# Optimization experiments

Hardware: AMD Instinct MI355X
Metric: run time of the kernel (lower is better)

Reference implementation:

```python
import jax, jax.numpy as jnp
import numpy as np

FD, FO, FK, H = 1024, 512, 128, 4
N = 32768


def setup_inputs() -> dict:
    key = jax.random.key(0)
    ks = jax.random.split(key, 8)
    s = 0.02
    return {
        "Xd": jax.random.normal(ks[0], (N, FD), dtype=jnp.float32),
        "Xo": jax.random.normal(ks[1], (N, FO), dtype=jnp.float32),
        "Wq": jax.random.normal(ks[2], (FO, FK * H), dtype=jnp.float32) * s,
        "bq": jnp.zeros((FK * H,), dtype=jnp.float32),
        "Wk": jax.random.normal(ks[3], (FD, FK * H), dtype=jnp.float32) * s,
        "bk": jnp.zeros((FK * H,), dtype=jnp.float32),
        "Wv": jax.random.normal(ks[4], (FD, FD * H), dtype=jnp.float32) * s,
        "bv": jnp.zeros((FD * H,), dtype=jnp.float32),
    }


def reference(Xd, Xo, Wq, bq, Wk, bk, Wv, bv):
    n = Xd.shape[0]
    Q = (Xo @ Wq + bq).reshape(n, H, FK)      # (n, H, fk)
    K = (Xd @ Wk + bk).reshape(n, H, FK)      # (n, H, fk)
    V = (Xd @ Wv + bv).reshape(n, H, FD)      # (n, H, fd)
    scores = jnp.sum(Q * K, axis=2, keepdims=True)  # (n, H, 1), no softmax
    Z = scores * V                              # (n, H, fd)
    Z = jnp.max(Z, axis=1)                      # max pooling over heads -> (n, fd)
    return Z  # dropout is identity in inference
```

## Files before the change

### kernel.cpp

```cpp
#include <hip/hip_runtime.h>

typedef __attribute__((ext_vector_type(8))) short short8;
typedef __attribute__((ext_vector_type(4))) float f32x4;

#define GLL16(gp, lp) __builtin_amdgcn_global_load_lds( \
    (__attribute__((address_space(1))) void*)(gp), \
    (__attribute__((address_space(3))) void*)(lp), 16, 0, 0)

__device__ __forceinline__ unsigned short f2b(float f) {
  unsigned int u = __builtin_bit_cast(unsigned int, f);
  u += 0x7fffu + ((u >> 16) & 1u);
  return (unsigned short)(u >> 16);
}
__device__ __forceinline__ float b2f(unsigned short s) {
  unsigned int u = ((unsigned int)s) << 16;
  return __builtin_bit_cast(float, u);
}

__global__ __launch_bounds__(256) void conv_k(const float* __restrict__ in,
                                              short8* __restrict__ out, long n8) {
  for (long i = (long)blockIdx.x * 256 + threadIdx.x; i < n8;
       i += (long)gridDim.x * 256) {
    const float4* p = (const float4*)in + 2 * i;
    float4 a = p[0], b = p[1];
    short8 v;
    v[0] = (short)f2b(a.x); v[1] = (short)f2b(a.y);
    v[2] = (short)f2b(a.z); v[3] = (short)f2b(a.w);
    v[4] = (short)f2b(b.x); v[5] = (short)f2b(b.y);
    v[6] = (short)f2b(b.z); v[7] = (short)f2b(b.w);
    out[i] = v;
  }
}

__global__ __launch_bounds__(256) void tconv_k(const float* __restrict__ in,
                                               unsigned short* __restrict__ out,
                                               int K, int C, int inter) {
  __shared__ float t[32][33];
  int k0 = blockIdx.x * 32, c0 = blockIdx.y * 32;
  int tx = threadIdx.x & 31, ty = threadIdx.x >> 5;
#pragma unroll
  for (int p = 0; p < 4; ++p)
    t[ty + p * 8][tx] = in[(size_t)(k0 + ty + p * 8) * C + c0 + tx];
  __syncthreads();
#pragma unroll
  for (int p = 0; p < 4; ++p) {
    int c = ty + p * 8;
    int gc = c0 + c;
    int orow = inter ? ((gc & 1023) * 4 + (gc >> 10)) : gc;
    out[(size_t)orow * K + k0 + tx] = f2b(t[tx][c]);
  }
}

template <int KD>
__global__ __launch_bounds__(512, 2) void gemm_v256_k(
    const unsigned short* __restrict__ A, const unsigned short* __restrict__ Bt,
    const float* __restrict__ bias, const float* __restrict__ sc,
    float* __restrict__ Z) {
  __shared__ __align__(16) char lds[65536];
  __shared__ float s_sc[1024];

  const int NKT = KD / 32;
  int tid = threadIdx.x;
  int bid = blockIdx.x;
  int cpx = gridDim.x >> 3;
  int lb = (bid & 7) * cpx + (bid >> 3);
  int mtile = lb >> 4, nt0 = lb & 15;
  long m0 = (long)mtile * 256;
  int l = tid & 63, wid = tid >> 6, wm = wid >> 2, wn = wid & 3;

  for (int i = tid; i < 1024; i += 512) s_sc[i] = sc[m0 * 4 + i];

  int srg = tid >> 3, slot = tid & 7;
  int se = slot ^ (srg & 7);
  int par = se >> 2, kc = se & 3;
  int rowb = srg * 2 + par;
  const char* aT = (const char*)(A + m0 * KD) + (long)rowb * (KD * 2) + kc * 16;
  const char* bT = (const char*)(Bt + (long)nt0 * 256 * KD) + (long)rowb * (KD * 2) + kc * 16;
  char* ldsb = (char*)lds;
  int dstOff = wid * 1024;

  auto stage = [&](int kt, int bb) {
    int ko = kt * 64;
    GLL16(aT + ko,                  ldsb + bb * 32768 + dstOff);
    GLL16(aT + 128 * (KD * 2) + ko, ldsb + bb * 32768 + 8192 + dstOff);
    GLL16(bT + ko,                  ldsb + bb * 32768 + 16384 + dstOff);
    GLL16(bT + 128 * (KD * 2) + ko, ldsb + bb * 32768 + 24576 + dstOff);
  };

  int ar = l & 15, kcl = l >> 4;
  int aoffR[8], boffR[4];
#pragma unroll
  for (int m = 0; m < 8; ++m) {
    int wr = wm * 128 + m * 16 + ar, sr = wr >> 1;
    aoffR[m] = sr * 128 + (((((wr & 1) << 2) | kcl) ^ (sr & 7)) << 4);
  }
#pragma unroll
  for (int n = 0; n < 4; ++n) {
    int br = wn * 64 + n * 16 + ar, sr = br >> 1;
    boffR[n] = sr * 128 + (((((br & 1) << 2) | kcl) ^ (sr & 7)) << 4);
  }

  f32x4 zero = {0.f, 0.f, 0.f, 0.f};
  f32x4 acc[8][4];
#pragma unroll
  for (int m = 0; m < 8; ++m)
#pragma unroll
    for (int n = 0; n < 4; ++n) acc[m][n] = zero;

  stage(0, 0);

  for (int t = 0; t < NKT; ++t) {
    asm volatile("s_waitcnt vmcnt(0)" ::: "memory");
    __builtin_amdgcn_s_barrier();
    asm volatile("" ::: "memory");
    if (t + 1 < NKT) stage(t + 1, (t + 1) & 1);

    const char* Al = ldsb + (t & 1) * 32768;
    const char* Bl = Al + 16384;
    short8 bf[4], af[4], af2[4];
#pragma unroll
    for (int n = 0; n < 4; ++n) bf[n] = *(const short8*)(Bl + boffR[n]);
#pragma unroll
    for (int m = 0; m < 4; ++m) af[m] = *(const short8*)(Al + aoffR[m]);
#pragma unroll
    for (int m = 0; m < 4; ++m) af2[m] = *(const short8*)(Al + aoffR[4 + m]);

#pragma unroll
    for (int m = 0; m < 4; ++m)
#pragma unroll
      for (int n = 0; n < 4; ++n)
        acc[m][n] = __builtin_amdgcn_mfma_f32_16x16x32_bf16(af[m], bf[n],
                                                            acc[m][n], 0, 0, 0);
#pragma unroll
    for (int m = 0; m < 4; ++m)
#pragma unroll
      for (int n = 0; n < 4; ++n)
        acc[4 + m][n] = __builtin_amdgcn_mfma_f32_16x16x32_bf16(af2[m], bf[n],
                                                                acc[4 + m][n], 0, 0, 0);
  }

  __syncthreads();
  float* Zs = (float*)ldsb;
#pragma unroll
  for (int n = 0; n < 4; ++n) {
    int pl = wn * 64 + n * 16 + (l & 15);
    int pg = nt0 * 256 + pl;
    int h = pl & 3;
    float bb = bias[(pg & 3) * 1024 + (pg >> 2)];
#pragma unroll
    for (int mi = 0; mi < 8; ++mi) {
      int rl = wm * 128 + mi * 16 + ((l >> 4) << 2);
#pragma unroll
      for (int r = 0; r < 4; ++r) {
        float z = s_sc[(rl + r) * 4 + h] * (acc[mi][n][r] + bb);
        z = fmaxf(z, __shfl_xor(z, 1));
        z = fmaxf(z, __shfl_xor(z, 2));
        if ((l & 3) == 0) Zs[(rl + r) * 64 + (pl >> 2)] = z;
      }
    }
  }
  __syncthreads();
#pragma unroll
  for (int it = 0; it < 8; ++it) {
    int i = it * 512 + tid;
    int row = i >> 4, d4 = i & 15;
    f32x4 v = *(const f32x4*)&Zs[row * 64 + d4 * 4];
    *(f32x4*)&Z[(m0 + row) * 1024 + nt0 * 64 + d4 * 4] = v;
  }
}

template <int KD, int EPI>
__global__ __launch_bounds__(256) void gemm_k(
    const unsigned short* __restrict__ A, const unsigned short* __restrict__ Bt,
    const float* __restrict__ bias, const unsigned short* __restrict__ Qb,
    unsigned short* __restrict__ outb, float* __restrict__ sc) {
  __shared__ __align__(16) unsigned short As[128 * 64];
  __shared__ __align__(16) unsigned short Bs[128 * 64];
  __shared__ float sred[128][2];

  int tid = threadIdx.x;
  int bid = blockIdx.x;
  int ntile = bid & 3, mtile = bid >> 2;
  int l = tid & 63, wid = tid >> 6, wm = wid >> 1, wn = wid & 1;
  int m0 = mtile * 128;

  const unsigned short* Ab = A + (size_t)m0 * KD;
  const unsigned short* Bb = Bt + (size_t)ntile * 128 * KD;

  f32x4 zero = {0.f, 0.f, 0.f, 0.f};
  f32x4 acc[4][4];
#pragma unroll
  for (int m = 0; m < 4; ++m)
#pragma unroll
    for (int n = 0; n < 4; ++n) acc[m][n] = zero;

  for (int kt = 0; kt < KD / 64; ++kt) {
    const unsigned short* sA = Ab + kt * 64;
    const unsigned short* sB = Bb + kt * 64;
#pragma unroll
    for (int p = 0; p < 4; ++p) {
      int row = p * 32 + wid * 8 + (l >> 3);
      int sch = (l & 7) ^ (row & 7);
      GLL16((const char*)(sA + (size_t)row * KD) + sch * 16,
            (char*)As + p * 4096 + wid * 1024);
    }
#pragma unroll
    for (int p = 0; p < 4; ++p) {
      int row = p * 32 + wid * 8 + (l >> 3);
      int sch = (l & 7) ^ (row & 7);
      GLL16((const char*)(sB + (size_t)row * KD) + sch * 16,
            (char*)Bs + p * 4096 + wid * 1024);
    }
    __syncthreads();
#pragma unroll
    for (int ks = 0; ks < 2; ++ks) {
      short8 af[4], bfr[4];
#pragma unroll
      for (int m = 0; m < 4; ++m) {
        int row = wm * 64 + m * 16 + (l & 15);
        int kc = ks * 4 + (l >> 4);
        af[m] = *(const short8*)((const char*)As + row * 128 +
                                 ((kc ^ (row & 7)) << 4));
      }
#pragma unroll
      for (int n = 0; n < 4; ++n) {
        int row = wn * 64 + n * 16 + (l & 15);
        int kc = ks * 4 + (l >> 4);
        bfr[n] = *(const short8*)((const char*)Bs + row * 128 +
                                  ((kc ^ (row & 7)) << 4));
      }
#pragma unroll
      for (int m = 0; m < 4; ++m)
#pragma unroll
        for (int n = 0; n < 4; ++n)
          acc[m][n] = __builtin_amdgcn_mfma_f32_16x16x32_bf16(af[m], bfr[n],
                                                              acc[m][n], 0, 0, 0);
    }
    __syncthreads();
  }

  if constexpr (EPI == 0) {
#pragma unroll
    for (int n = 0; n < 4; ++n) {
      int col = ntile * 128 + wn * 64 + n * 16 + (l & 15);
      float bb = bias[col];
#pragma unroll
      for (int m = 0; m < 4; ++m) {
        int rowb = m0 + wm * 64 + m * 16 + ((l >> 4) << 2);
#pragma unroll
        for (int r = 0; r < 4; ++r)
          outb[(size_t)(rowb + r) * 512 + col] = f2b(acc[m][n][r] + bb);
      }
    }
  } else {
    float part[4][4] = {};
#pragma unroll
    for (int n = 0; n < 4; ++n) {
      int col = ntile * 128 + wn * 64 + n * 16 + (l & 15);
      float bb = bias[col];
#pragma unroll
      for (int m = 0; m < 4; ++m) {
        int rowb = m0 + wm * 64 + m * 16 + ((l >> 4) << 2);
#pragma unroll
        for (int r = 0; r < 4; ++r) {
          float kv = acc[m][n][r] + bb;
          part[m][r] += kv * b2f(Qb[(size_t)(rowb + r) * 512 + col]);
        }
      }
    }
#pragma unroll
    for (int m = 0; m < 4; ++m)
#pragma unroll
      for (int r = 0; r < 4; ++r) {
        float s = part[m][r];
        s += __shfl_xor(s, 1);
        s += __shfl_xor(s, 2);
        s += __shfl_xor(s, 4);
        s += __shfl_xor(s, 8);
        if ((l & 15) == 0)
          sred[wm * 64 + m * 16 + ((l >> 4) << 2) + r][wn] = s;
      }
    __syncthreads();
    if (tid < 128) sc[(size_t)(m0 + tid) * 4 + ntile] = sred[tid][0] + sred[tid][1];
  }
}

__global__ __launch_bounds__(256) void naive_k(
    const float* __restrict__ Xd, const float* __restrict__ Xo,
    const float* __restrict__ Wq, const float* __restrict__ bq,
    const float* __restrict__ Wk, const float* __restrict__ bk,
    const float* __restrict__ Wv, const float* __restrict__ bv,
    float* __restrict__ Z) {
  int i = blockIdx.x, t = threadIdx.x;
  __shared__ float xd[1024], xo[512], s[4];
  for (int j = t; j < 1024; j += 256) xd[j] = Xd[(size_t)i * 1024 + j];
  for (int j = t; j < 512; j += 256) xo[j] = Xo[(size_t)i * 512 + j];
  if (t < 4) s[t] = 0.f;
  __syncthreads();
  for (int c = t; c < 512; c += 256) {
    float q = bq[c], k = bk[c];
    for (int j = 0; j < 512; ++j) q += xo[j] * Wq[(size_t)j * 512 + c];
    for (int j = 0; j < 1024; ++j) k += xd[j] * Wk[(size_t)j * 512 + c];
    atomicAdd(&s[c >> 7], q * k);
  }
  __syncthreads();
  for (int d = t; d < 1024; d += 256) {
    float z = -INFINITY;
    for (int h = 0; h < 4; ++h) {
      float v = bv[h * 1024 + d];
      for (int j = 0; j < 1024; ++j) v += xd[j] * Wv[(size_t)j * 4096 + h * 1024 + d];
      z = fmaxf(z, s[h] * v);
    }
    Z[(size_t)i * 1024 + d] = z;
  }
}

extern "C" void kernel_launch(void* const* d_in, const int* in_sizes, int n_in,
                              void* d_out, int out_size, void* d_ws, size_t ws_size,
                              hipStream_t stream) {
  const float* Xd = (const float*)d_in[0];
  const float* Xo = (const float*)d_in[1];
  const float* Wq = (const float*)d_in[2];
  const float* bq = (const float*)d_in[3];
  const float* Wk = (const float*)d_in[4];
  const float* bk = (const float*)d_in[5];
  const float* Wv = (const float*)d_in[6];
  const float* bv = (const float*)d_in[7];
  float* Z = (float*)d_out;
  long N = in_sizes[0] / 1024;

  size_t sz_Xd = (size_t)N * 1024 * 2, sz_Xo = (size_t)N * 512 * 2;
  size_t sz_Wq = (size_t)512 * 512 * 2, sz_Wk = (size_t)512 * 1024 * 2;
  size_t sz_Wv = (size_t)4096 * 1024 * 2;
  size_t sz_Qb = (size_t)N * 512 * 2, sz_sc = (size_t)N * 4 * 4;
  size_t o_Xo = sz_Xd, o_Wq = o_Xo + sz_Xo, o_Wk = o_Wq + sz_Wq,
         o_Wv = o_Wk + sz_Wk, o_Qb = o_Wv + sz_Wv, o_sc = o_Qb + sz_Qb;
  size_t need = o_sc + sz_sc;

  if (ws_size < need || (N % 256) != 0) {
    naive_k<<<(int)N, 256, 0, stream>>>(Xd, Xo, Wq, bq, Wk, bk, Wv, bv, Z);
    return;
  }

  char* w = (char*)d_ws;
  unsigned short* Xd_b = (unsigned short*)w;
  unsigned short* Xo_b = (unsigned short*)(w + o_Xo);
  unsigned short* Wq_t = (unsigned short*)(w + o_Wq);
  unsigned short* Wk_t = (unsigned short*)(w + o_Wk);
  unsigned short* Wv_p = (unsigned short*)(w + o_Wv);
  unsigned short* Qb   = (unsigned short*)(w + o_Qb);
  float* sc = (float*)(w + o_sc);

  conv_k<<<2048, 256, 0, stream>>>(Xd, (short8*)Xd_b, N * 1024 / 8);
  conv_k<<<2048, 256, 0, stream>>>(Xo, (short8*)Xo_b, N * 512 / 8);
  tconv_k<<<dim3(16, 16), 256, 0, stream>>>(Wq, Wq_t, 512, 512, 0);
  tconv_k<<<dim3(32, 16), 256, 0, stream>>>(Wk, Wk_t, 1024, 512, 0);
  tconv_k<<<dim3(32, 128), 256, 0, stream>>>(Wv, Wv_p, 1024, 4096, 1);

  int mt = (int)(N / 128);
  gemm_k<512, 0><<<mt * 4, 256, 0, stream>>>(Xo_b, Wq_t, bq, nullptr, Qb, nullptr);
  gemm_k<1024, 1><<<mt * 4, 256, 0, stream>>>(Xd_b, Wk_t, bk, Qb, nullptr, sc);
  gemm_v256_k<1024><<<(int)(N / 256) * 16, 512, 0, stream>>>(Xd_b, Wv_p, bv, sc, Z);
}
```

Measured before the change: 553.8 us.

## Restructure V GEMM into 8-wave ping-pong with quadrant pipelining and BK=64

Rewrites the dominant V-projection GEMM kernel. The K tile grows to 64 and LDS to 128KB, split into A/B halves. The 256x256 output is computed as four 128x128 quadrants, with global-to-LDS loads for the next tile interleaved between quadrant MFMA phases under barriers and s_setprio. The aim is to hide memory latency behind MFMA work and halve the number of K-loop iterations. The cost is more barriers per iteration and doubled LDS, which limits occupancy to one block per CU despite the launch bound of 2.

```diff
diff --git a/kernel.cpp b/kernel.cpp
--- a/kernel.cpp
+++ b/kernel.cpp
@@ -52,14 +52,14 @@
 }
 
 template <int KD>
-__global__ __launch_bounds__(512, 2) void gemm_v256_k(
+__global__ __launch_bounds__(512, 2) void gemm_v8p(
     const unsigned short* __restrict__ A, const unsigned short* __restrict__ Bt,
     const float* __restrict__ bias, const float* __restrict__ sc,
     float* __restrict__ Z) {
-  __shared__ __align__(16) char lds[65536];
+  __shared__ __align__(16) char lds[131072];
   __shared__ float s_sc[1024];
 
-  const int NKT = KD / 32;
+  constexpr int NKT = KD / 64;
   int tid = threadIdx.x;
   int bid = blockIdx.x;
   int cpx = gridDim.x >> 3;
@@ -70,95 +70,140 @@
 
   for (int i = tid; i < 1024; i += 512) s_sc[i] = sc[m0 * 4 + i];
 
-  int srg = tid >> 3, slot = tid & 7;
-  int se = slot ^ (srg & 7);
-  int par = se >> 2, kc = se & 3;
-  int rowb = srg * 2 + par;
-  const char* aT = (const char*)(A + m0 * KD) + (long)rowb * (KD * 2) + kc * 16;
-  const char* bT = (const char*)(Bt + (long)nt0 * 256 * KD) + (long)rowb * (KD * 2) + kc * 16;
+  int rowg = tid >> 3;
+  int swz = (tid & 7) ^ (rowg & 7);
+  const char* aSrc = (const char*)(A + m0 * KD) + (long)rowg * (KD * 2) + swz * 16;
+  const char* bSrc = (const char*)(Bt + (long)nt0 * 256 * KD) + (long)rowg * (KD * 2) + swz * 16;
   char* ldsb = (char*)lds;
   int dstOff = wid * 1024;
 
-  auto stage = [&](int kt, int bb) {
-    int ko = kt * 64;
-    GLL16(aT + ko,                  ldsb + bb * 32768 + dstOff);
-    GLL16(aT + 128 * (KD * 2) + ko, ldsb + bb * 32768 + 8192 + dstOff);
-    GLL16(bT + ko,                  ldsb + bb * 32768 + 16384 + dstOff);
-    GLL16(bT + 128 * (KD * 2) + ko, ldsb + bb * 32768 + 24576 + dstOff);
+  auto stageA = [&](int hh, int tt) {
+    char* base = ldsb + (((tt & 1) * 2 + hh) * 16384) + dstOff;
+    const char* s = aSrc + (long)(hh * 128) * (KD * 2) + tt * 128;
+    GLL16(s, base);
+    GLL16(s + (long)64 * (KD * 2), base + 8192);
   };
+  auto stageB = [&](int hh, int tt) {
+    char* base = ldsb + 65536 + (((tt & 1) * 2 + hh) * 16384) + dstOff;
+    const char* s = bSrc + (long)(hh * 128) * (KD * 2) + tt * 128;
+    GLL16(s, base);
+    GLL16(s + (long)64 * (KD * 2), base + 8192);
+  };
 
   int ar = l & 15, kcl = l >> 4;
-  int aoffR[8], boffR[4];
-#pragma unroll
-  for (int m = 0; m < 8; ++m) {
-    int wr = wm * 128 + m * 16 + ar, sr = wr >> 1;
-    aoffR[m] = sr * 128 + (((((wr & 1) << 2) | kcl) ^ (sr & 7)) << 4);
-  }
-#pragma unroll
-  for (int n = 0; n < 4; ++n) {
-    int br = wn * 64 + n * 16 + ar, sr = br >> 1;
-    boffR[n] = sr * 128 + (((((br & 1) << 2) | kcl) ^ (sr & 7)) << 4);
+  int aoff[4][2], boff[2][2];
+#pragma unroll
+  for (int m = 0; m < 4; ++m) {
+    int lrow = wm * 64 + m * 16 + ar;
+#pragma unroll
+    for (int ks = 0; ks < 2; ++ks)
+      aoff[m][ks] = lrow * 128 + (((ks * 4 + kcl) ^ (lrow & 7)) << 4);
+  }
+#pragma unroll
+  for (int n = 0; n < 2; ++n) {
+    int lcol = wn * 32 + n * 16 + ar;
+#pragma unroll
+    for (int ks = 0; ks < 2; ++ks)
+      boff[n][ks] = lcol * 128 + (((ks * 4 + kcl) ^ (lcol & 7)) << 4);
   }
 
   f32x4 zero = {0.f, 0.f, 0.f, 0.f};
-  f32x4 acc[8][4];
-#pragma unroll
-  for (int m = 0; m < 8; ++m)
-#pragma unroll
-    for (int n = 0; n < 4; ++n) acc[m][n] = zero;
-
-  stage(0, 0);
+  f32x4 acc[4][8];
+#pragma unroll
+  for (int q = 0; q < 4; ++q)
+#pragma unroll
+    for (int f = 0; f < 8; ++f) acc[q][f] = zero;
+
+  short8 a[4][2], b0[2][2], b1[2][2];
+
+#define READ_A(slotbase)                                                   \
+  _Pragma("unroll") for (int m_ = 0; m_ < 4; ++m_)                         \
+      _Pragma("unroll") for (int k_ = 0; k_ < 2; ++k_)                     \
+          a[m_][k_] = *(const short8*)((slotbase) + aoff[m_][k_]);
+#define READ_B(dst, slotbase)                                              \
+  _Pragma("unroll") for (int n_ = 0; n_ < 2; ++n_)                         \
+      _Pragma("unroll") for (int k_ = 0; k_ < 2; ++k_)                     \
+          dst[n_][k_] = *(const short8*)((slotbase) + boff[n_][k_]);
+#define MFMA_Q(q, bq)                                                      \
+  __builtin_amdgcn_s_setprio(1);                                           \
+  _Pragma("unroll") for (int m_ = 0; m_ < 4; ++m_)                         \
+      _Pragma("unroll") for (int n_ = 0; n_ < 2; ++n_)                     \
+          _Pragma("unroll") for (int k_ = 0; k_ < 2; ++k_)                 \
+              acc[q][m_ * 2 + n_] = __builtin_amdgcn_mfma_f32_16x16x32_bf16( \
+                  a[m_][k_], bq[n_][k_], acc[q][m_ * 2 + n_], 0, 0, 0);    \
+  __builtin_amdgcn_s_setprio(0);
+#define WAITV()                                                            \
+  if (t < NKT - 1) { asm volatile("s_waitcnt vmcnt(4)" ::: "memory"); }    \
+  else             { asm volatile("s_waitcnt vmcnt(0)" ::: "memory"); }
+#define BAR() __builtin_amdgcn_s_barrier()
+#define LGKM0() asm volatile("s_waitcnt lgkmcnt(0)" ::: "memory")
+
+  stageA(0, 0); stageB(0, 0); stageB(1, 0); stageA(1, 0);
+  asm volatile("s_waitcnt vmcnt(4)" ::: "memory");
+  BAR();
 
   for (int t = 0; t < NKT; ++t) {
-    asm volatile("s_waitcnt vmcnt(0)" ::: "memory");
-    __builtin_amdgcn_s_barrier();
-    asm volatile("" ::: "memory");
-    if (t + 1 < NKT) stage(t + 1, (t + 1) & 1);
-
-    const char* Al = ldsb + (t & 1) * 32768;
-    const char* Bl = Al + 16384;
-    short8 bf[4], af[4], af2[4];
-#pragma unroll
-    for (int n = 0; n < 4; ++n) bf[n] = *(const short8*)(Bl + boffR[n]);
-#pragma unroll
-    for (int m = 0; m < 4; ++m) af[m] = *(const short8*)(Al + aoffR[m]);
-#pragma unroll
-    for (int m = 0; m < 4; ++m) af2[m] = *(const short8*)(Al + aoffR[4 + m]);
-
-#pragma unroll
-    for (int m = 0; m < 4; ++m)
-#pragma unroll
-      for (int n = 0; n < 4; ++n)
-        acc[m][n] = __builtin_amdgcn_mfma_f32_16x16x32_bf16(af[m], bf[n],
-                                                            acc[m][n], 0, 0, 0);
-#pragma unroll
-    for (int m = 0; m < 4; ++m)
-#pragma unroll
-      for (int n = 0; n < 4; ++n)
-        acc[4 + m][n] = __builtin_amdgcn_mfma_f32_16x16x32_bf16(af2[m], bf[n],
-                                                                acc[4 + m][n], 0, 0, 0);
-  }
+    char* aS = ldsb + ((t & 1) * 2) * 16384;
+    char* bS = ldsb + 65536 + ((t & 1) * 2) * 16384;
+    bool st = (t + 1 < NKT);
+
+    READ_A(aS);
+    READ_B(b0, bS);
+    if (st) stageA(0, t + 1);
+    WAITV(); BAR(); LGKM0();
+    MFMA_Q(0, b0);
+    BAR();
+
+    READ_B(b1, bS + 16384);
+    if (st) stageB(0, t + 1);
+    WAITV(); BAR(); LGKM0();
+    MFMA_Q(1, b1);
+    BAR();
+
+    READ_A(aS + 16384);
+    if (st) stageB(1, t + 1);
+    WAITV(); BAR(); LGKM0();
+    MFMA_Q(2, b0);
+    BAR();
+
+    if (st) stageA(1, t + 1);
+    WAITV(); BAR();
+    MFMA_Q(3, b1);
+    BAR();
+  }
+#undef READ_A
+#undef READ_B
+#undef MFMA_Q
+#undef WAITV
+#undef BAR
+#undef LGKM0
 
   __syncthreads();
   float* Zs = (float*)ldsb;
 #pragma unroll
-  for (int n = 0; n < 4; ++n) {
-    int pl = wn * 64 + n * 16 + (l & 15);
-    int pg = nt0 * 256 + pl;
-    int h = pl & 3;
-    float bb = bias[(pg & 3) * 1024 + (pg >> 2)];
-#pragma unroll
-    for (int mi = 0; mi < 8; ++mi) {
-      int rl = wm * 128 + mi * 16 + ((l >> 4) << 2);
-#pragma unroll
-      for (int r = 0; r < 4; ++r) {
-        float z = s_sc[(rl + r) * 4 + h] * (acc[mi][n][r] + bb);
-        z = fmaxf(z, __shfl_xor(z, 1));
-        z = fmaxf(z, __shfl_xor(z, 2));
-        if ((l & 3) == 0) Zs[(rl + r) * 64 + (pl >> 2)] = z;
-      }
-    }
-  }
+  for (int qm = 0; qm < 2; ++qm)
+#pragma unroll
+    for (int qn = 0; qn < 2; ++qn) {
+      int q = qm * 2 + qn;
+#pragma unroll
+      for (int n = 0; n < 2; ++n) {
+        int pl = qn * 128 + wn * 32 + n * 16 + (l & 15);
+        int pg = nt0 * 256 + pl;
+        int h = pl & 3;
+        float bb = bias[(pg & 3) * 1024 + (pg >> 2)];
+#pragma unroll
+        for (int m = 0; m < 4; ++m) {
+          int rl = qm * 128 + wm * 64 + m * 16 + ((l >> 4) << 2);
+#pragma unroll
+          for (int r = 0; r < 4; ++r) {
+            float z = s_sc[(rl + r) * 4 + h] * (acc[q][m * 2 + n][r] + bb);
+            z = fmaxf(z, __shfl_xor(z, 1));
+            z = fmaxf(z, __shfl_xor(z, 2));
+            if ((l & 3) == 0) Zs[(rl + r) * 64 + (pl >> 2)] = z;
+          }
+        }
+      }
+    }
   __syncthreads();
 #pragma unroll
   for (int it = 0; it < 8; ++it) {
@@ -360,5 +405,5 @@
   int mt = (int)(N / 128);
   gemm_k<512, 0><<<mt * 4, 256, 0, stream>>>(Xo_b, Wq_t, bq, nullptr, Qb, nullptr);
   gemm_k<1024, 1><<<mt * 4, 256, 0, stream>>>(Xd_b, Wk_t, bk, Qb, nullptr, sc);
-  gemm_v256_k<1024><<<(int)(N / 256) * 16, 512, 0, stream>>>(Xd_b, Wv_p, bv, sc, Z);
-}
+  gemm_v8p<1024><<<(int)(N / 256) * 16, 512, 0, stream>>>(Xd_b, Wv_p, bv, sc, Z);
+}
```

Result: faster. 477.2 us (-13.8%).
